# Performance work log

Hardware: AMD Instinct MI355X
Metric: run time of the kernel (lower is better)

Reference implementation:

```python
import jax, jax.numpy as jnp
import numpy as np

B, S, NH, HD = 2, 2048, 32, 128     # batch seqs, tokens per seq, heads, head_dim
H = NH * HD                          # hidden = 4096
BLOCK = 64                           # paged KV-cache block size
NBLK = S // BLOCK                    # blocks per sequence
NUM_BLOCKS = B * NBLK                # total cache blocks


def alibi_slopes(n):
    # n is a power of two: slope_i = 2^(-8*(i+1)/n)
    return np.asarray([2.0 ** (-8.0 * (i + 1) / n) for i in range(n)], dtype=np.float32)


def setup_inputs() -> dict:
    key = jax.random.key(0)
    k1, k2, k3 = jax.random.split(key, 3)
    hidden_states = jax.random.normal(k1, (B * S, H), jnp.float32)
    w_pack = jax.random.normal(k2, (H, 3 * H), jnp.float32) * 0.02
    o_proj_w = jax.random.normal(k3, (H, H), jnp.float32) * 0.02
    k_cache = jnp.zeros((NUM_BLOCKS, BLOCK, NH, HD), jnp.float32)
    v_cache = jnp.zeros((NUM_BLOCKS, BLOCK, NH, HD), jnp.float32)
    block_offsets = jnp.arange(NUM_BLOCKS, dtype=jnp.int32).reshape(B, NBLK)
    return {
        "hidden_states": hidden_states,
        "w_pack": w_pack,
        "o_proj_w": o_proj_w,
        "k_cache": k_cache,
        "v_cache": v_cache,
        "block_offsets": block_offsets,
    }


def reference(hidden_states, w_pack, o_proj_w, k_cache, v_cache, block_offsets):
    # fused QKV projection, chunk(3, -1)
    qkv = hidden_states @ w_pack                      # [B*S, 3H]
    q, k, v = jnp.split(qkv, 3, axis=-1)
    q = q.reshape(B, S, NH, HD)
    k = k.reshape(B, NBLK, BLOCK, NH, HD)
    v = v.reshape(B, NBLK, BLOCK, NH, HD)

    # fill_kv_cache: scatter new K/V into paged cache blocks
    k_cache = k_cache.at[block_offsets].set(k)        # [NUM_BLOCKS, BLOCK, NH, HD]
    v_cache = v_cache.at[block_offsets].set(v)

    # paged read: gather non-contiguous blocks back per sequence
    kg = k_cache[block_offsets].reshape(B, S, NH, HD)
    vg = v_cache[block_offsets].reshape(B, S, NH, HD)

    slopes = jnp.asarray(alibi_slopes(NH))            # [NH]
    scale = 1.0 / jnp.sqrt(jnp.float32(HD))
    scores = jnp.einsum('bqhd,bkhd->bhqk', q, kg) * scale   # [B,NH,S,S]
    pos = jnp.arange(S)
    # ALiBi bias: slope * key_position (row-shift invariant under softmax)
    scores = scores + slopes[None, :, None, None] * pos[None, None, None, :]
    causal = pos[:, None] >= pos[None, :]             # [S,S]
    scores = jnp.where(causal[None, None], scores, jnp.float32(-1e30))
    probs = jax.nn.softmax(scores, axis=-1)
    attn = jnp.einsum('bhqk,bkhd->bqhd', probs, vg).reshape(B * S, H)
    return attn @ o_proj_w
```

## Files before the change

### kernel.cpp

```cpp
#include <hip/hip_runtime.h>
#include <hip/hip_bf16.h>
#include <stdint.h>

typedef __attribute__((ext_vector_type(4))) float f32x4;
typedef __attribute__((ext_vector_type(8))) __bf16 bf16x8;
typedef __attribute__((ext_vector_type(8))) unsigned short u16x8;
typedef __attribute__((ext_vector_type(4))) unsigned short u16x4;
typedef __attribute__((ext_vector_type(2))) unsigned int u32x2;
typedef __attribute__((ext_vector_type(4))) unsigned int u32x4;

#define GLL16(g, l) __builtin_amdgcn_global_load_lds( \
    (const __attribute__((address_space(1))) unsigned int*)(uintptr_t)(g), \
    (__attribute__((address_space(3))) unsigned int*)(uintptr_t)(l), 16, 0, 0)

__device__ __forceinline__ unsigned short bf16u(float f) {
  return __builtin_bit_cast(unsigned short, __float2bfloat16(f));
}

#define PB 2
#define PS 2048
#define PNH 32
#define PHD 128
#define PH 4096
#define P3H 12288

__global__ __launch_bounds__(256)
void cvt_f32_bf16(const float* __restrict__ in, unsigned short* __restrict__ out, int n) {
  int stride = gridDim.x * blockDim.x;
  for (int i = blockIdx.x * blockDim.x + threadIdx.x; i * 8 < n; i += stride) {
    int base = i * 8;
    f32x4 a = *(const f32x4*)(in + base);
    f32x4 b = *(const f32x4*)(in + base + 4);
    u16x8 o;
#pragma unroll
    for (int j = 0; j < 4; ++j) { o[j] = bf16u(a[j]); o[4 + j] = bf16u(b[j]); }
    *(u16x8*)(out + base) = o;
  }
}

__global__ __launch_bounds__(256)
void transpose_cvt(const float* __restrict__ in, unsigned short* __restrict__ out,
                   int K, int N) {
  __shared__ __align__(16) unsigned short tile[64][68];
  int k0 = blockIdx.y * 64, n0 = blockIdx.x * 64;
  int t = threadIdx.x;
  int rr = t >> 4, cc = (t & 15) * 4;
#pragma unroll
  for (int p = 0; p < 4; ++p) {
    int r = rr + p * 16;
    f32x4 v = *(const f32x4*)(in + (size_t)(k0 + r) * N + n0 + cc);
    u16x4 w;
#pragma unroll
    for (int j = 0; j < 4; ++j) w[j] = bf16u(v[j]);
    *(u16x4*)&tile[r][cc] = w;
  }
  __syncthreads();
#pragma unroll
  for (int p = 0; p < 4; ++p) {
    int nl = rr + p * 16;
    u16x4 w;
#pragma unroll
    for (int j = 0; j < 4; ++j) w[j] = tile[cc + j][nl];
    *(u16x4*)(out + (size_t)(n0 + nl) * K + k0 + cc) = w;
  }
}

#define STAGE_A(TT) do { int sb_ = ((TT) & 3) << 15; \
    GLL16(aSrc0 + (size_t)(TT) * 32, smem + sb_ + (wave << 10)); \
    GLL16(aSrc1 + (size_t)(TT) * 32, smem + sb_ + 8192 + (wave << 10)); } while (0)
#define STAGE_B(TT) do { int sb_ = ((TT) & 3) << 15; \
    GLL16(bSrc0 + (size_t)(TT) * 32, smem + sb_ + 16384 + (wave << 10)); \
    GLL16(bSrc1 + (size_t)(TT) * 32, smem + sb_ + 24576 + (wave << 10)); } while (0)

#define TILEBODY(T, DOSTAGE, VM) do { \
    char* AsB_ = smem + (((T) & 3) << 15); \
    char* BsB_ = AsB_ + 16384; \
    bf16x8 av[4], bv[4]; \
    _Pragma("unroll") \
    for (int i = 0; i < 4; ++i) \
      av[i] = *(const bf16x8*)(AsB_ + (((wm << 7) + (i << 4) + lr) << 6) + lchunk); \
    _Pragma("unroll") \
    for (int j = 0; j < 4; ++j) \
      bv[j] = *(const bf16x8*)(BsB_ + (((wn << 6) + (j << 4) + lr) << 6) + lchunk); \
    if (DOSTAGE) { STAGE_A((T) + 2); } \
    __builtin_amdgcn_s_barrier(); \
    __builtin_amdgcn_s_setprio(1); \
    _Pragma("unroll") \
    for (int i = 0; i < 4; ++i) \
      _Pragma("unroll") \
      for (int j = 0; j < 4; ++j) \
        acc[i][j] = __builtin_amdgcn_mfma_f32_16x16x32_bf16(av[i], bv[j], acc[i][j], 0, 0, 0); \
    __builtin_amdgcn_s_setprio(0); \
    __builtin_amdgcn_s_barrier(); \
    _Pragma("unroll") \
    for (int i = 0; i < 4; ++i) \
      av[i] = *(const bf16x8*)(AsB_ + (((wm << 7) + 64 + (i << 4) + lr) << 6) + lchunk); \
    if (DOSTAGE) { STAGE_B((T) + 2); } \
    __builtin_amdgcn_s_barrier(); \
    __builtin_amdgcn_s_setprio(1); \
    _Pragma("unroll") \
    for (int i = 0; i < 4; ++i) \
      _Pragma("unroll") \
      for (int j = 0; j < 4; ++j) \
        acc[4 + i][j] = __builtin_amdgcn_mfma_f32_16x16x32_bf16(av[i], bv[j], acc[4 + i][j], 0, 0, 0); \
    __builtin_amdgcn_s_setprio(0); \
    if ((VM) == 4)      asm volatile("s_waitcnt vmcnt(4)" ::: "memory"); \
    else if ((VM) == 0) asm volatile("s_waitcnt vmcnt(0)" ::: "memory"); \
    __builtin_amdgcn_s_barrier(); \
  } while (0)

template<int OUTF32>
__global__ __launch_bounds__(512, 2)
void gemm256(const unsigned short* __restrict__ A, const unsigned short* __restrict__ Bt,
             void* __restrict__ Cv, int M, int N, int K) {
  __shared__ __align__(16) char smem[131072];
  const int tid = threadIdx.x;
  const int wave = tid >> 6, lane = tid & 63;
  const int lr = lane & 15, lg = lane >> 4;
  const int wm = wave >> 2, wn = wave & 3;
  const int lchunk = (lg ^ ((lr >> 1) & 3)) << 4;
  const int nbn = N >> 8;
  const int nwg = (M >> 8) * nbn;
  int bid = blockIdx.x;
  int qq = nwg >> 3;
  int wg = (bid & 7) * qq + (bid >> 3);
  int bm = wg / nbn, bn = wg % nbn;
  const size_t arow = (size_t)bm << 8;
  const size_t brow = (size_t)bn << 8;

  const int srow = (wave << 4) + (lane >> 2);
  const int scol = ((lane & 3) ^ ((lane >> 3) & 3)) << 3;
  const unsigned short* aSrc0 = A  + (arow + srow) * K + scol;
  const unsigned short* aSrc1 = A  + (arow + 128 + srow) * K + scol;
  const unsigned short* bSrc0 = Bt + (brow + srow) * K + scol;
  const unsigned short* bSrc1 = Bt + (brow + 128 + srow) * K + scol;

  f32x4 acc[8][4] = {};

  STAGE_A(0); STAGE_B(0); STAGE_A(1); STAGE_B(1);
  asm volatile("s_waitcnt vmcnt(4)" ::: "memory");
  __builtin_amdgcn_s_barrier();

  const int NT = K >> 5;
  for (int t = 0; t < NT - 2; ++t) TILEBODY(t, 1, 4);
  TILEBODY(NT - 2, 0, 0);
  TILEBODY(NT - 1, 0, -1);

  int crow = (bm << 8) + (wm << 7) + (lg << 2);
  int ccol = (bn << 8) + (wn << 6) + lr;
#pragma unroll
  for (int i = 0; i < 8; ++i)
#pragma unroll
    for (int j = 0; j < 4; ++j)
#pragma unroll
      for (int r = 0; r < 4; ++r) {
        size_t off = (size_t)(crow + (i << 4) + r) * N + ccol + (j << 4);
        if (OUTF32) ((float*)Cv)[off] = acc[i][j][r];
        else        ((unsigned short*)Cv)[off] = bf16u(acc[i][j][r]);
      }
}

__global__ __launch_bounds__(256, 2)
void attn_kernel(const unsigned short* __restrict__ qkv, unsigned short* __restrict__ out) {
  __shared__ __align__(16) unsigned short Ks[2][64 * 128];
  __shared__ __align__(16) unsigned short Vt[128 * 64];
  __shared__ __align__(16) unsigned short Ps[4][16 * 88];
  int tid = threadIdx.x, wave = tid >> 6, lane = tid & 63;
  int lr = lane & 15, lg = lane >> 4;
  int idx = blockIdx.x;
  int qt = 31 - (idx & 31);
  int h = (idx >> 5) & 31, b = idx >> 10;
  size_t rb = (size_t)b * PS;
  int qcol = h << 7, kcol = PH + (h << 7), vcol = 2 * PH + (h << 7);
  int q0 = (qt << 6) + (wave << 4);

  bf16x8 aq[4];
#pragma unroll
  for (int f = 0; f < 4; ++f)
    aq[f] = *(const bf16x8*)(qkv + (rb + q0 + lr) * P3H + qcol + (f << 5) + (lg << 3));

  float m_run[4] = {-1e30f, -1e30f, -1e30f, -1e30f};
  float l_run[4] = {0.f, 0.f, 0.f, 0.f};
  f32x4 acc_o[8] = {};

  float slope2 = __builtin_amdgcn_exp2f(-(float)(h + 1) * 0.25f) * 1.44269504f;
  const float scale2 = 0.08838834764831845f * 1.44269504f;

  char* KsB = (char*)Ks;
  char* VtB = (char*)Vt;
  const int kk0 = (tid & 15) << 2, d0 = (tid >> 4) << 3;

  {
    size_t krow = rb;
#pragma unroll
    for (int i = 0; i < 4; ++i) {
      int pf = (wave << 12) | (i << 10) | (lane << 4);
      int row = pf >> 8;
      int lch = ((pf >> 4) & 15) ^ (row & 7);
      GLL16(qkv + (krow + row) * P3H + kcol + (lch << 3), KsB + (wave << 12) + (i << 10));
    }
  }
  u32x4 vr0 = *(const u32x4*)(qkv + (rb + kk0 + 0) * P3H + vcol + d0);
  u32x4 vr1 = *(const u32x4*)(qkv + (rb + kk0 + 1) * P3H + vcol + d0);
  u32x4 vr2 = *(const u32x4*)(qkv + (rb + kk0 + 2) * P3H + vcol + d0);
  u32x4 vr3 = *(const u32x4*)(qkv + (rb + kk0 + 3) * P3H + vcol + d0);

  for (int t = 0; t <= qt; ++t) {
    int cur = t & 1;
    char* KsCur = KsB + (cur << 14);
    char* KsNxt = KsB + ((cur ^ 1) << 14);
    bool more = (t < qt);

    u32x4 nv0 = {}, nv1 = {}, nv2 = {}, nv3 = {};
    if (more) {
      size_t krow = rb + ((size_t)(t + 1) << 6);
#pragma unroll
      for (int i = 0; i < 4; ++i) {
        int pf = (wave << 12) | (i << 10) | (lane << 4);
        int row = pf >> 8;
        int lch = ((pf >> 4) & 15) ^ (row & 7);
        GLL16(qkv + (krow + row) * P3H + kcol + (lch << 3), KsNxt + (wave << 12) + (i << 10));
      }
      nv0 = *(const u32x4*)(qkv + (krow + kk0 + 0) * P3H + vcol + d0);
      nv1 = *(const u32x4*)(qkv + (krow + kk0 + 1) * P3H + vcol + d0);
      nv2 = *(const u32x4*)(qkv + (krow + kk0 + 2) * P3H + vcol + d0);
      nv3 = *(const u32x4*)(qkv + (krow + kk0 + 3) * P3H + vcol + d0);
    }

    if (more) asm volatile("s_waitcnt vmcnt(8)" ::: "memory");
    else      asm volatile("s_waitcnt vmcnt(0)" ::: "memory");

    {
      const unsigned short* e0 = (const unsigned short*)&vr0;
      const unsigned short* e1 = (const unsigned short*)&vr1;
      const unsigned short* e2 = (const unsigned short*)&vr2;
      const unsigned short* e3 = (const unsigned short*)&vr3;
#pragma unroll
      for (int j = 0; j < 8; ++j) {
        int d = d0 + j;
        u32x2 w;
        w.x = (unsigned int)e0[j] | ((unsigned int)e1[j] << 16);
        w.y = (unsigned int)e2[j] | ((unsigned int)e3[j] << 16);
        int byteoff = ((d << 7) + (kk0 << 1)) ^ ((d & 7) << 4);
        *(u32x2*)(VtB + byteoff) = w;
      }
    }
    asm volatile("s_waitcnt lgkmcnt(0)" ::: "memory");
    __builtin_amdgcn_s_barrier();

    f32x4 sc[4];
    __builtin_amdgcn_s_setprio(1);
#pragma unroll
    for (int f = 0; f < 4; ++f) {
      f32x4 c = {};
#pragma unroll
      for (int ks = 0; ks < 4; ++ks) {
        int kkr = (f << 4) + lr;
        int ch = (lg + (ks << 2)) ^ (kkr & 7);
        bf16x8 bk = *(const bf16x8*)(KsCur + (kkr << 8) + (ch << 4));
        c = __builtin_amdgcn_mfma_f32_16x16x32_bf16(aq[ks], bk, c, 0, 0, 0);
      }
      sc[f] = c;
    }
    __builtin_amdgcn_s_setprio(0);

    int kvb = t << 6;
    bool lastt = (t == qt);
    float vals[4][4];
#pragma unroll
    for (int f = 0; f < 4; ++f) {
      int kv = kvb + (f << 4) + lr;
      float bias = slope2 * (float)kv;
#pragma unroll
      for (int r = 0; r < 4; ++r) {
        float v = sc[f][r] * scale2 + bias;
        if (lastt && kv > q0 + (lg << 2) + r) v = -1e30f;
        vals[r][f] = v;
      }
    }
    float alpha[4];
#pragma unroll
    for (int r = 0; r < 4; ++r) {
      float mr = fmaxf(fmaxf(vals[r][0], vals[r][1]), fmaxf(vals[r][2], vals[r][3]));
#pragma unroll
      for (int d2 = 1; d2 < 16; d2 <<= 1) mr = fmaxf(mr, __shfl_xor(mr, d2, 16));
      float mnew = fmaxf(m_run[r], mr);
      alpha[r] = __builtin_amdgcn_exp2f(m_run[r] - mnew);
      m_run[r] = mnew;
    }
#pragma unroll
    for (int r = 0; r < 4; ++r) {
      float s = 0.f;
#pragma unroll
      for (int f = 0; f < 4; ++f) {
        float p = __builtin_amdgcn_exp2f(vals[r][f] - m_run[r]);
        s += p;
        Ps[wave][((lg << 2) + r) * 88 + (f << 4) + lr] = bf16u(p);
      }
      l_run[r] = l_run[r] * alpha[r] + s;
    }
#pragma unroll
    for (int d = 0; d < 8; ++d) {
      f32x4 a4 = acc_o[d];
#pragma unroll
      for (int r = 0; r < 4; ++r) a4[r] *= alpha[r];
      acc_o[d] = a4;
    }

    bf16x8 pa[2];
#pragma unroll
    for (int ks = 0; ks < 2; ++ks)
      pa[ks] = *(const bf16x8*)((char*)&Ps[wave][0] + lr * 176 + (ks << 6) + (lg << 4));
    __builtin_amdgcn_s_setprio(1);
#pragma unroll
    for (int d = 0; d < 8; ++d) {
#pragma unroll
      for (int ks = 0; ks < 2; ++ks) {
        int dr = (d << 4) + lr;
        int ch = (lg + (ks << 2)) ^ (dr & 7);
        bf16x8 bv = *(const bf16x8*)(VtB + (dr << 7) + (ch << 4));
        acc_o[d] = __builtin_amdgcn_mfma_f32_16x16x32_bf16(pa[ks], bv, acc_o[d], 0, 0, 0);
      }
    }
    __builtin_amdgcn_s_setprio(0);
    __builtin_amdgcn_s_barrier();

    if (more) { vr0 = nv0; vr1 = nv1; vr2 = nv2; vr3 = nv3; }
  }

  float rinv[4];
#pragma unroll
  for (int r = 0; r < 4; ++r) {
    float s = l_run[r];
#pragma unroll
    for (int d2 = 1; d2 < 16; d2 <<= 1) s += __shfl_xor(s, d2, 16);
    rinv[r] = 1.f / s;
  }
#pragma unroll
  for (int d = 0; d < 8; ++d)
#pragma unroll
    for (int r = 0; r < 4; ++r) {
      float o = acc_o[d][r] * rinv[r];
      out[(rb + q0 + (lg << 2) + r) * PH + (h << 7) + (d << 4) + lr] = bf16u(o);
    }
}

extern "C" void kernel_launch(void* const* d_in, const int* in_sizes, int n_in,
                              void* d_out, int out_size, void* d_ws, size_t ws_size,
                              hipStream_t stream) {
  const float* hidden = (const float*)d_in[0];
  const float* w_pack = (const float*)d_in[1];
  const float* o_proj = (const float*)d_in[2];

  char* ws = (char*)d_ws;
  unsigned short* wpackT = (unsigned short*)(ws);
  unsigned short* qkv    = (unsigned short*)(ws + 100663296);
  unsigned short* oprojT = (unsigned short*)(ws + 201326592);
  unsigned short* hbf    = (unsigned short*)(ws + 234881024);
  unsigned short* attnb  = hbf;

  int M = PB * PS;

  cvt_f32_bf16<<<2048, 256, 0, stream>>>(hidden, hbf, M * PH);
  transpose_cvt<<<dim3(P3H / 64, PH / 64), 256, 0, stream>>>(w_pack, wpackT, PH, P3H);
  transpose_cvt<<<dim3(PH / 64, PH / 64), 256, 0, stream>>>(o_proj, oprojT, PH, PH);
  gemm256<0><<<(M / 256) * (P3H / 256), 512, 0, stream>>>(hbf, wpackT, qkv, M, P3H, PH);
  attn_kernel<<<PB * PNH * (PS / 64), 256, 0, stream>>>(qkv, attnb);
  gemm256<1><<<(M / 256) * (PH / 256), 512, 0, stream>>>(attnb, oprojT, d_out, M, PH, PH);
}
```

Measured before the change: 884.5 us.

## Process 128 query rows per attention block, two 16-row subtiles per wave

The attention kernel now gives each workgroup a 128-row query tile, and each wave handles two 16-row query subtiles. Every K/V tile staged in shared memory is reused by twice as many queries, which halves K/V global traffic and staging work per query. The causal mask now applies to any KV tile overlapping the wave's rows instead of only the last one. In exchange the grid is halved, which costs parallelism and worsens causal load imbalance, and per-thread register use for accumulators and softmax state roughly doubles, which may lower occupancy.

```diff
diff --git a/kernel.cpp b/kernel.cpp
--- a/kernel.cpp
+++ b/kernel.cpp
@@ -164,24 +164,29 @@
 void attn_kernel(const unsigned short* __restrict__ qkv, unsigned short* __restrict__ out) {
   __shared__ __align__(16) unsigned short Ks[2][64 * 128];
   __shared__ __align__(16) unsigned short Vt[128 * 64];
-  __shared__ __align__(16) unsigned short Ps[4][16 * 88];
+  __shared__ __align__(16) unsigned short Ps[4][32 * 88];
   int tid = threadIdx.x, wave = tid >> 6, lane = tid & 63;
   int lr = lane & 15, lg = lane >> 4;
   int idx = blockIdx.x;
-  int qt = 31 - (idx & 31);
-  int h = (idx >> 5) & 31, b = idx >> 10;
+  int qt = 15 - (idx & 15);
+  int h = (idx >> 4) & 31, b = idx >> 9;
   size_t rb = (size_t)b * PS;
   int qcol = h << 7, kcol = PH + (h << 7), vcol = 2 * PH + (h << 7);
-  int q0 = (qt << 6) + (wave << 4);
-
-  bf16x8 aq[4];
-#pragma unroll
-  for (int f = 0; f < 4; ++f)
-    aq[f] = *(const bf16x8*)(qkv + (rb + q0 + lr) * P3H + qcol + (f << 5) + (lg << 3));
-
-  float m_run[4] = {-1e30f, -1e30f, -1e30f, -1e30f};
-  float l_run[4] = {0.f, 0.f, 0.f, 0.f};
-  f32x4 acc_o[8] = {};
+  int q0 = (qt << 7) + (wave << 5);
+
+  bf16x8 aq[2][4];
+#pragma unroll
+  for (int qs = 0; qs < 2; ++qs)
+#pragma unroll
+    for (int f = 0; f < 4; ++f)
+      aq[qs][f] = *(const bf16x8*)(qkv + (rb + q0 + (qs << 4) + lr) * P3H + qcol + (f << 5) + (lg << 3));
+
+  float m_run[2][4], l_run[2][4];
+#pragma unroll
+  for (int qs = 0; qs < 2; ++qs)
+#pragma unroll
+    for (int r = 0; r < 4; ++r) { m_run[qs][r] = -1e30f; l_run[qs][r] = 0.f; }
+  f32x4 acc_o[2][8] = {};
 
   float slope2 = __builtin_amdgcn_exp2f(-(float)(h + 1) * 0.25f) * 1.44269504f;
   const float scale2 = 0.08838834764831845f * 1.44269504f;
@@ -205,11 +210,12 @@
   u32x4 vr2 = *(const u32x4*)(qkv + (rb + kk0 + 2) * P3H + vcol + d0);
   u32x4 vr3 = *(const u32x4*)(qkv + (rb + kk0 + 3) * P3H + vcol + d0);
 
-  for (int t = 0; t <= qt; ++t) {
+  const int tmax = 2 * qt + 1;
+  for (int t = 0; t <= tmax; ++t) {
     int cur = t & 1;
     char* KsCur = KsB + (cur << 14);
     char* KsNxt = KsB + ((cur ^ 1) << 14);
-    bool more = (t < qt);
+    bool more = (t < tmax);
 
     u32x4 nv0 = {}, nv1 = {}, nv2 = {}, nv3 = {};
     if (more) {
@@ -248,69 +254,75 @@
     asm volatile("s_waitcnt lgkmcnt(0)" ::: "memory");
     __builtin_amdgcn_s_barrier();
 
-    f32x4 sc[4];
+    f32x4 sc[2][4];
     __builtin_amdgcn_s_setprio(1);
 #pragma unroll
     for (int f = 0; f < 4; ++f) {
-      f32x4 c = {};
+      f32x4 c0 = {}, c1 = {};
 #pragma unroll
       for (int ks = 0; ks < 4; ++ks) {
         int kkr = (f << 4) + lr;
         int ch = (lg + (ks << 2)) ^ (kkr & 7);
         bf16x8 bk = *(const bf16x8*)(KsCur + (kkr << 8) + (ch << 4));
-        c = __builtin_amdgcn_mfma_f32_16x16x32_bf16(aq[ks], bk, c, 0, 0, 0);
-      }
-      sc[f] = c;
+        c0 = __builtin_amdgcn_mfma_f32_16x16x32_bf16(aq[0][ks], bk, c0, 0, 0, 0);
+        c1 = __builtin_amdgcn_mfma_f32_16x16x32_bf16(aq[1][ks], bk, c1, 0, 0, 0);
+      }
+      sc[0][f] = c0; sc[1][f] = c1;
     }
     __builtin_amdgcn_s_setprio(0);
 
     int kvb = t << 6;
-    bool lastt = (t == qt);
-    float vals[4][4];
-#pragma unroll
-    for (int f = 0; f < 4; ++f) {
-      int kv = kvb + (f << 4) + lr;
-      float bias = slope2 * (float)kv;
+    bool needmask = (kvb + 63 > q0);
+#pragma unroll
+    for (int qs = 0; qs < 2; ++qs) {
+      float vals[4][4];
+#pragma unroll
+      for (int f = 0; f < 4; ++f) {
+        int kv = kvb + (f << 4) + lr;
+        float bias = slope2 * (float)kv;
+#pragma unroll
+        for (int r = 0; r < 4; ++r) {
+          float v = sc[qs][f][r] * scale2 + bias;
+          if (needmask && kv > q0 + (qs << 4) + (lg << 2) + r) v = -1e30f;
+          vals[r][f] = v;
+        }
+      }
+      float alpha[4];
 #pragma unroll
       for (int r = 0; r < 4; ++r) {
-        float v = sc[f][r] * scale2 + bias;
-        if (lastt && kv > q0 + (lg << 2) + r) v = -1e30f;
-        vals[r][f] = v;
-      }
-    }
-    float alpha[4];
-#pragma unroll
-    for (int r = 0; r < 4; ++r) {
-      float mr = fmaxf(fmaxf(vals[r][0], vals[r][1]), fmaxf(vals[r][2], vals[r][3]));
-#pragma unroll
-      for (int d2 = 1; d2 < 16; d2 <<= 1) mr = fmaxf(mr, __shfl_xor(mr, d2, 16));
-      float mnew = fmaxf(m_run[r], mr);
-      alpha[r] = __builtin_amdgcn_exp2f(m_run[r] - mnew);
-      m_run[r] = mnew;
-    }
-#pragma unroll
-    for (int r = 0; r < 4; ++r) {
-      float s = 0.f;
-#pragma unroll
-      for (int f = 0; f < 4; ++f) {
-        float p = __builtin_amdgcn_exp2f(vals[r][f] - m_run[r]);
-        s += p;
-        Ps[wave][((lg << 2) + r) * 88 + (f << 4) + lr] = bf16u(p);
-      }
-      l_run[r] = l_run[r] * alpha[r] + s;
-    }
-#pragma unroll
-    for (int d = 0; d < 8; ++d) {
-      f32x4 a4 = acc_o[d];
-#pragma unroll
-      for (int r = 0; r < 4; ++r) a4[r] *= alpha[r];
-      acc_o[d] = a4;
-    }
-
-    bf16x8 pa[2];
-#pragma unroll
-    for (int ks = 0; ks < 2; ++ks)
-      pa[ks] = *(const bf16x8*)((char*)&Ps[wave][0] + lr * 176 + (ks << 6) + (lg << 4));
+        float mr = fmaxf(fmaxf(vals[r][0], vals[r][1]), fmaxf(vals[r][2], vals[r][3]));
+#pragma unroll
+        for (int d2 = 1; d2 < 16; d2 <<= 1) mr = fmaxf(mr, __shfl_xor(mr, d2, 16));
+        float mnew = fmaxf(m_run[qs][r], mr);
+        alpha[r] = __builtin_amdgcn_exp2f(m_run[qs][r] - mnew);
+        m_run[qs][r] = mnew;
+      }
+#pragma unroll
+      for (int r = 0; r < 4; ++r) {
+        float s = 0.f;
+#pragma unroll
+        for (int f = 0; f < 4; ++f) {
+          float p = __builtin_amdgcn_exp2f(vals[r][f] - m_run[qs][r]);
+          s += p;
+          Ps[wave][((qs << 4) + (lg << 2) + r) * 88 + (f << 4) + lr] = bf16u(p);
+        }
+        l_run[qs][r] = l_run[qs][r] * alpha[r] + s;
+      }
+#pragma unroll
+      for (int d = 0; d < 8; ++d) {
+        f32x4 a4 = acc_o[qs][d];
+#pragma unroll
+        for (int r = 0; r < 4; ++r) a4[r] *= alpha[r];
+        acc_o[qs][d] = a4;
+      }
+    }
+
+    bf16x8 pa[2][2];
+#pragma unroll
+    for (int qs = 0; qs < 2; ++qs)
+#pragma unroll
+      for (int ks = 0; ks < 2; ++ks)
+        pa[qs][ks] = *(const bf16x8*)((char*)&Ps[wave][0] + ((qs << 4) + lr) * 176 + (ks << 6) + (lg << 4));
     __builtin_amdgcn_s_setprio(1);
 #pragma unroll
     for (int d = 0; d < 8; ++d) {
@@ -319,7 +331,8 @@
         int dr = (d << 4) + lr;
         int ch = (lg + (ks << 2)) ^ (dr & 7);
         bf16x8 bv = *(const bf16x8*)(VtB + (dr << 7) + (ch << 4));
-        acc_o[d] = __builtin_amdgcn_mfma_f32_16x16x32_bf16(pa[ks], bv, acc_o[d], 0, 0, 0);
+        acc_o[0][d] = __builtin_amdgcn_mfma_f32_16x16x32_bf16(pa[0][ks], bv, acc_o[0][d], 0, 0, 0);
+        acc_o[1][d] = __builtin_amdgcn_mfma_f32_16x16x32_bf16(pa[1][ks], bv, acc_o[1][d], 0, 0, 0);
       }
     }
     __builtin_amdgcn_s_setprio(0);
@@ -328,21 +341,24 @@
     if (more) { vr0 = nv0; vr1 = nv1; vr2 = nv2; vr3 = nv3; }
   }
 
-  float rinv[4];
-#pragma unroll
-  for (int r = 0; r < 4; ++r) {
-    float s = l_run[r];
-#pragma unroll
-    for (int d2 = 1; d2 < 16; d2 <<= 1) s += __shfl_xor(s, d2, 16);
-    rinv[r] = 1.f / s;
-  }
-#pragma unroll
-  for (int d = 0; d < 8; ++d)
+#pragma unroll
+  for (int qs = 0; qs < 2; ++qs) {
+    float rinv[4];
 #pragma unroll
     for (int r = 0; r < 4; ++r) {
-      float o = acc_o[d][r] * rinv[r];
-      out[(rb + q0 + (lg << 2) + r) * PH + (h << 7) + (d << 4) + lr] = bf16u(o);
-    }
+      float s = l_run[qs][r];
+#pragma unroll
+      for (int d2 = 1; d2 < 16; d2 <<= 1) s += __shfl_xor(s, d2, 16);
+      rinv[r] = 1.f / s;
+    }
+#pragma unroll
+    for (int d = 0; d < 8; ++d)
+#pragma unroll
+      for (int r = 0; r < 4; ++r) {
+        float o = acc_o[qs][d][r] * rinv[r];
+        out[(rb + q0 + (qs << 4) + (lg << 2) + r) * PH + (h << 7) + (d << 4) + lr] = bf16u(o);
+      }
+  }
 }
 
 extern "C" void kernel_launch(void* const* d_in, const int* in_sizes, int n_in,
@@ -365,6 +381,6 @@
   transpose_cvt<<<dim3(P3H / 64, PH / 64), 256, 0, stream>>>(w_pack, wpackT, PH, P3H);
   transpose_cvt<<<dim3(PH / 64, PH / 64), 256, 0, stream>>>(o_proj, oprojT, PH, PH);
   gemm256<0><<<(M / 256) * (P3H / 256), 512, 0, stream>>>(hbf, wpackT, qkv, M, P3H, PH);
-  attn_kernel<<<PB * PNH * (PS / 64), 256, 0, stream>>>(qkv, attnb);
+  attn_kernel<<<PB * PNH * (PS / 128), 256, 0, stream>>>(qkv, attnb);
   gemm256<1><<<(M / 256) * (PH / 256), 512, 0, stream>>>(attnb, oprojT, d_out, M, PH, PH);
 }
```

Result: faster. 858.5 us (-2.9%).
